# Optimization experiments

Hardware: AMD Instinct MI355X
Metric: run time of the kernel (lower is better)

The kernel has to match this reference:

```python
import jax, jax.numpy as jnp
import numpy as np

EPS = 1e-5
GROUPS = 32

def _group_norm(x, w, b):
    N, C, H, W = x.shape
    g = GROUPS
    xr = x.reshape(N, g, C // g, H, W)
    mean = xr.mean(axis=(2, 3, 4), keepdims=True)
    var = xr.var(axis=(2, 3, 4), keepdims=True)
    xn = ((xr - mean) / jnp.sqrt(var + EPS)).reshape(N, C, H, W)
    return xn * w[None, :, None, None] + b[None, :, None, None]

def setup_inputs() -> dict:
    key = jax.random.key(0)
    ks = jax.random.split(key, 9)
    N, C, H, W = 8, 256, 64, 64
    c = C // 2
    s_in = 1.0 / np.sqrt(C)
    s_out = 1.0 / np.sqrt(c)
    return {
        "x": jax.random.normal(ks[0], (N, C, H, W), dtype=jnp.float32),
        "gn_w": jnp.ones((C,), dtype=jnp.float32),
        "gn_b": jnp.zeros((C,), dtype=jnp.float32),
        "wq": jax.random.normal(ks[1], (c, C), dtype=jnp.float32) * s_in,
        "bq": jax.random.normal(ks[2], (c,), dtype=jnp.float32) * 0.01,
        "wk": jax.random.normal(ks[3], (c, C), dtype=jnp.float32) * s_in,
        "bk": jax.random.normal(ks[4], (c,), dtype=jnp.float32) * 0.01,
        "wv": jax.random.normal(ks[5], (c, C), dtype=jnp.float32) * s_in,
        "bv": jax.random.normal(ks[6], (c,), dtype=jnp.float32) * 0.01,
        "wo": jax.random.normal(ks[7], (C, c), dtype=jnp.float32) * s_out,
        "bo": jax.random.normal(ks[8], (C,), dtype=jnp.float32) * 0.01,
    }

def reference(x, gn_w, gn_b, wq, bq, wk, bk, wv, bv, wo, bo):
    N, C, H, W = x.shape
    c = C // 2
    L = H * W
    f = jax.nn.silu(_group_norm(x, gn_w, gn_b))  # [N,C,H,W]
    fv = f.reshape(N, C, L)  # [N,C,L]
    q = jnp.einsum('oc,ncl->nol', wq, fv) + bq[None, :, None]  # [N,c,L]
    k = jnp.einsum('oc,ncl->nol', wk, fv) + bk[None, :, None]
    v = jnp.einsum('oc,ncl->nol', wv, fv) + bv[None, :, None]
    e = jnp.einsum('nci,ncj->nij', q, k)          # [N,L,L] (no scaling, as in source)
    a = jax.nn.softmax(e, axis=-1)
    f2 = jnp.einsum('ncj,nij->nci', v, a)          # [N,c,L]
    out = jnp.einsum('oc,ncl->nol', wo, jax.nn.silu(f2)) + bo[None, :, None]
    return out.reshape(N, C, H, W) + x
```

## Files before the change

### kernel.cpp

```cpp
#include <hip/hip_runtime.h>

typedef _Float16 f16;
typedef _Float16 f16x8 __attribute__((ext_vector_type(8)));
typedef float f32x4 __attribute__((ext_vector_type(4)));

static constexpr int N_ = 8, C_ = 256, c_ = 128, L_ = 4096;

#define DEVI __device__ __forceinline__

DEVI f16x8 ldg8(const f16* p){ return *reinterpret_cast<const f16x8*>(p); }
DEVI f32x4 mfma16(f16x8 a, f16x8 b, f32x4 c){
  return __builtin_amdgcn_mfma_f32_16x16x32_f16(a, b, c, 0, 0, 0);
}
DEVI float silu(float x){ return x / (1.f + __expf(-x)); }

__global__ __launch_bounds__(256) void prep_weights(const float* __restrict__ wq,
    const float* __restrict__ wk, const float* __restrict__ wv,
    const float* __restrict__ wo, f16* __restrict__ dst){
  int i = blockIdx.x * 256 + threadIdx.x;
  int off = i & 32767;
  const float* s;
  switch (i >> 15){
    case 0:  s = wq; break;
    case 1:  s = wk; break;
    case 2:  s = wv; break;
    default: s = wo; break;
  }
  dst[i] = (f16)s[off];
}

__global__ __launch_bounds__(256) void gn_stats(const float* __restrict__ x,
                                                float* __restrict__ st){
  int n = blockIdx.x >> 5, g = blockIdx.x & 31;
  const float* base = x + (size_t)(n * C_ + g * 8) * L_;
  float s = 0.f, ss = 0.f;
  for (int it = 0; it < 32; ++it){
    float4 v = *reinterpret_cast<const float4*>(base + it * 1024 + threadIdx.x * 4);
    s  += v.x + v.y + v.z + v.w;
    ss += v.x * v.x + v.y * v.y + v.z * v.z + v.w * v.w;
  }
  #pragma unroll
  for (int m = 1; m <= 32; m <<= 1){ s += __shfl_xor(s, m); ss += __shfl_xor(ss, m); }
  __shared__ float red[8];
  int w = threadIdx.x >> 6;
  if ((threadIdx.x & 63) == 0){ red[w] = s; red[4 + w] = ss; }
  __syncthreads();
  if (threadIdx.x == 0){
    s  = red[0] + red[1] + red[2] + red[3];
    ss = red[4] + red[5] + red[6] + red[7];
    float mean = s * (1.f / 32768.f);
    float var  = ss * (1.f / 32768.f) - mean * mean;
    float2 o; o.x = mean; o.y = rsqrtf(var + 1e-5f);
    reinterpret_cast<float2*>(st)[blockIdx.x] = o;
  }
}

__global__ __launch_bounds__(256) void gn_apply(const float* __restrict__ x,
    const float* __restrict__ st, const float* __restrict__ gw,
    const float* __restrict__ gb, f16* __restrict__ fT){
  int n = blockIdx.z, c0 = blockIdx.y * 64, l0 = blockIdx.x * 64;
  __shared__ f16 tile[64][72];
  int t = threadIdx.x;
  int cr = t >> 4, lc = (t & 15) * 4;
  const float* xb = x + (size_t)(n * C_ + c0) * L_ + l0;
  #pragma unroll
  for (int p = 0; p < 4; ++p){
    int cc = cr + p * 16;
    int ch = c0 + cc;
    float2 ms = reinterpret_cast<const float2*>(st)[n * 32 + (ch >> 3)];
    float w = gw[ch], b = gb[ch];
    float4 v = *reinterpret_cast<const float4*>(xb + (size_t)cc * L_ + lc);
    float f0 = (v.x - ms.x) * ms.y * w + b;
    float f1 = (v.y - ms.x) * ms.y * w + b;
    float f2 = (v.z - ms.x) * ms.y * w + b;
    float f3 = (v.w - ms.x) * ms.y * w + b;
    tile[cc][lc + 0] = (f16)silu(f0);
    tile[cc][lc + 1] = (f16)silu(f1);
    tile[cc][lc + 2] = (f16)silu(f2);
    tile[cc][lc + 3] = (f16)silu(f3);
  }
  __syncthreads();
  int lr = t >> 2, cq = (t & 3) * 16;
  f16 tmp[16];
  #pragma unroll
  for (int e = 0; e < 16; ++e) tmp[e] = tile[cq + e][lr];
  f16* o = fT + (size_t)(n * L_ + l0 + lr) * C_ + c0 + cq;
  *reinterpret_cast<f16x8*>(o)     = *reinterpret_cast<f16x8*>(tmp);
  *reinterpret_cast<f16x8*>(o + 8) = *reinterpret_cast<f16x8*>(tmp + 8);
}

template<int EPI>
__global__ __launch_bounds__(256) void proj(const f16* __restrict__ A, size_t a_nstr,
    const f16* __restrict__ B, size_t b_nstr, const float* __restrict__ bias,
    void* __restrict__ outv, size_t o_nstr, int ldo,
    const float* __restrict__ resid, size_t r_nstr, int Ks,
    const float* __restrict__ bias2, void* __restrict__ outv2){
  int n = blockIdx.z;
  int i0 = blockIdx.x * 64;
  int w  = threadIdx.x >> 6;
  int jw = blockIdx.y * 128 + w * 32;
  int lane = threadIdx.x & 63, l15 = lane & 15, g4 = lane >> 4;
  const f16* Ab = A + (size_t)n * a_nstr;
  const f16* Bb = B + (size_t)n * b_nstr;
  int K = Ks * 32;
  f32x4 acc[4][2];
  #pragma unroll
  for (int mf = 0; mf < 4; ++mf)
    #pragma unroll
    for (int nf = 0; nf < 2; ++nf) acc[mf][nf] = (f32x4){0.f, 0.f, 0.f, 0.f};

  for (int ks = 0; ks < Ks; ++ks){
    int kk = ks * 32 + 8 * g4;
    f16x8 a[4], b[2];
    #pragma unroll
    for (int mf = 0; mf < 4; ++mf)
      a[mf] = ldg8(Ab + (size_t)(i0 + 16 * mf + l15) * K + kk);
    #pragma unroll
    for (int nf = 0; nf < 2; ++nf)
      b[nf] = ldg8(Bb + (size_t)(jw + 16 * nf + l15) * K + kk);
    #pragma unroll
    for (int mf = 0; mf < 4; ++mf)
      #pragma unroll
      for (int nf = 0; nf < 2; ++nf)
        acc[mf][nf] = mfma16(a[mf], b[nf], acc[mf][nf]);
  }

  #pragma unroll
  for (int mf = 0; mf < 4; ++mf){
    #pragma unroll
    for (int nf = 0; nf < 2; ++nf){
      int j = jw + 16 * nf + l15;
      #pragma unroll
      for (int r = 0; r < 4; ++r){
        int i = i0 + 16 * mf + 4 * g4 + r;
        float v = acc[mf][nf][r];
        if (EPI == 1){
          ((f16*)outv)[(size_t)n * o_nstr + (size_t)i * ldo + j] = (f16)(v + bias[i]);
        } else if (EPI == 2){
          size_t oidx = (size_t)n * o_nstr + (size_t)i * ldo + j;
          ((float*)outv)[oidx] = v + bias[i] + resid[(size_t)n * r_nstr + (size_t)i * ldo + j];
        } else {
          if (j < 128)
            ((f16*)outv)[(size_t)n * o_nstr + (size_t)i * ldo + j] = (f16)(v + bias[j]);
          else
            ((f16*)outv2)[(size_t)n * o_nstr + (size_t)i * ldo + (j - 128)] = (f16)(v + bias2[j - 128]);
        }
      }
    }
  }
}

__global__ __launch_bounds__(256) void flash(const f16* __restrict__ Qg,
    const f16* __restrict__ Kg, const f16* __restrict__ Vg, f16* __restrict__ Og){
  __shared__ char Ksh[16384];
  __shared__ char Vsh[16384];
  __shared__ char Psh[8192];
  int n = blockIdx.y;
  int q0 = blockIdx.x * 64;
  int tid = threadIdx.x;
  int w = tid >> 6, lane = tid & 63, l15 = lane & 15, g4 = lane >> 4;
  int qb = q0 + w * 16;

  const f16* Qn = Qg + (size_t)n * L_ * 128;
  const f16* Kn = Kg + (size_t)n * L_ * 128;
  const f16* Vn = Vg + (size_t)n * 128 * L_;

  f16x8 qf[4];
  #pragma unroll
  for (int ks = 0; ks < 4; ++ks)
    qf[ks] = ldg8(Qn + (size_t)(qb + l15) * 128 + ks * 32 + 8 * g4);

  f32x4 o[8];
  #pragma unroll
  for (int nf = 0; nf < 8; ++nf) o[nf] = (f32x4){0.f, 0.f, 0.f, 0.f};
  float mrow[4], lrow[4];
  #pragma unroll
  for (int r = 0; r < 4; ++r){ mrow[r] = -1e30f; lrow[r] = 0.f; }

  for (int t = 0; t < 64; ++t){
    #pragma unroll
    for (int it = 0; it < 4; ++it){
      int cid = it * 256 + tid;
      int j = cid >> 4, c16 = cid & 15;
      float4 val = *reinterpret_cast<const float4*>(Kn + (size_t)(t * 64 + j) * 128 + c16 * 8);
      *reinterpret_cast<float4*>(Ksh + j * 256 + ((c16 * 16) ^ ((j & 7) << 4))) = val;
    }
    #pragma unroll
    for (int it = 0; it < 4; ++it){
      int cid = it * 256 + tid;
      int d = cid >> 3, c16 = cid & 7;
      float4 val = *reinterpret_cast<const float4*>(Vn + (size_t)d * L_ + t * 64 + c16 * 8);
      *reinterpret_cast<float4*>(Vsh + d * 128 + ((c16 * 16) ^ ((d & 7) << 4))) = val;
    }
    __syncthreads();

    f32x4 s[4];
    #pragma unroll
    for (int nf = 0; nf < 4; ++nf) s[nf] = (f32x4){0.f, 0.f, 0.f, 0.f};
    #pragma unroll
    for (int ks = 0; ks < 4; ++ks){
      #pragma unroll
      for (int nf = 0; nf < 4; ++nf){
        int j = 16 * nf + l15;
        f16x8 kf = *reinterpret_cast<const f16x8*>(Ksh + j * 256 + ((64 * ks + 16 * g4) ^ ((j & 7) << 4)));
        s[nf] = mfma16(qf[ks], kf, s[nf]);
      }
    }

    float scl[4];
    #pragma unroll
    for (int r = 0; r < 4; ++r){
      float pm = fmaxf(fmaxf(s[0][r], s[1][r]), fmaxf(s[2][r], s[3][r]));
      pm = fmaxf(pm, __shfl_xor(pm, 1));
      pm = fmaxf(pm, __shfl_xor(pm, 2));
      pm = fmaxf(pm, __shfl_xor(pm, 4));
      pm = fmaxf(pm, __shfl_xor(pm, 8));
      float mnew = fmaxf(mrow[r], pm);
      scl[r] = __expf(mrow[r] - mnew);
      mrow[r] = mnew;
    }
    #pragma unroll
    for (int nf = 0; nf < 4; ++nf)
      #pragma unroll
      for (int r = 0; r < 4; ++r)
        s[nf][r] = __expf(s[nf][r] - mrow[r]);
    #pragma unroll
    for (int r = 0; r < 4; ++r){
      float rs = s[0][r] + s[1][r] + s[2][r] + s[3][r];
      rs += __shfl_xor(rs, 1);
      rs += __shfl_xor(rs, 2);
      rs += __shfl_xor(rs, 4);
      rs += __shfl_xor(rs, 8);
      lrow[r] = lrow[r] * scl[r] + rs;
    }
    #pragma unroll
    for (int nf = 0; nf < 8; ++nf)
      #pragma unroll
      for (int r = 0; r < 4; ++r)
        o[nf][r] *= scl[r];

    char* pb = Psh + w * 2048;
    #pragma unroll
    for (int nf = 0; nf < 4; ++nf)
      #pragma unroll
      for (int r = 0; r < 4; ++r){
        int i = 4 * g4 + r;
        int jj = 16 * nf + l15;
        *reinterpret_cast<f16*>(pb + i * 128 + ((2 * jj) ^ ((i & 7) << 4))) = (f16)s[nf][r];
      }

    #pragma unroll
    for (int ks = 0; ks < 2; ++ks){
      f16x8 pa = *reinterpret_cast<const f16x8*>(pb + l15 * 128 + ((64 * ks + 16 * g4) ^ ((l15 & 7) << 4)));
      #pragma unroll
      for (int nf = 0; nf < 8; ++nf){
        int d = 16 * nf + l15;
        f16x8 vf = *reinterpret_cast<const f16x8*>(Vsh + d * 128 + ((64 * ks + 16 * g4) ^ ((d & 7) << 4)));
        o[nf] = mfma16(pa, vf, o[nf]);
      }
    }
    __syncthreads();
  }

  f16* Ob = Og + (size_t)n * L_ * 128;
  #pragma unroll
  for (int r = 0; r < 4; ++r){
    float inv = 1.f / lrow[r];
    #pragma unroll
    for (int nf = 0; nf < 8; ++nf){
      float val = o[nf][r] * inv;
      Ob[(size_t)(qb + 4 * g4 + r) * 128 + 16 * nf + l15] = (f16)silu(val);
    }
  }
}

extern "C" void kernel_launch(void* const* d_in, const int* in_sizes, int n_in,
                              void* d_out, int out_size, void* d_ws, size_t ws_size,
                              hipStream_t stream){
  const float* x   = (const float*)d_in[0];
  const float* gnw = (const float*)d_in[1];
  const float* gnb = (const float*)d_in[2];
  const float* wq  = (const float*)d_in[3];
  const float* bq  = (const float*)d_in[4];
  const float* wk  = (const float*)d_in[5];
  const float* bk  = (const float*)d_in[6];
  const float* wv  = (const float*)d_in[7];
  const float* bv  = (const float*)d_in[8];
  const float* wo  = (const float*)d_in[9];
  const float* bo  = (const float*)d_in[10];
  float* out = (float*)d_out;

  char* ws = (char*)d_ws;
  f16* fT   = (f16*)(ws);
  f16* q    = (f16*)(ws + ((size_t)16 << 20));
  f16* k    = (f16*)(ws + ((size_t)24 << 20));
  f16* v    = (f16*)(ws + ((size_t)32 << 20));
  f16* gbuf = (f16*)(ws + ((size_t)40 << 20));
  f16* wh   = (f16*)(ws + ((size_t)48 << 20));
  float* st = (float*)(ws + ((size_t)49 << 20));

  prep_weights<<<512, 256, 0, stream>>>(wq, wk, wv, wo, wh);
  gn_stats<<<256, 256, 0, stream>>>(x, st);
  gn_apply<<<dim3(64, 4, 8), 256, 0, stream>>>(x, st, gnw, gnb, fT);

  proj<3><<<dim3(64, 2, 8), 256, 0, stream>>>(fT, (size_t)L_ * C_, wh, 0, bq,
                                              q, (size_t)L_ * c_, c_, nullptr, 0, 8, bk, k);
  proj<1><<<dim3(2, 32, 8), 256, 0, stream>>>(wh + 65536, 0, fT, (size_t)L_ * C_, bv,
                                              v, (size_t)c_ * L_, L_, nullptr, 0, 8, nullptr, nullptr);
  flash<<<dim3(64, 8), 256, 0, stream>>>(q, k, v, gbuf);
  proj<2><<<dim3(4, 32, 8), 256, 0, stream>>>(wh + 98304, 0, gbuf, (size_t)L_ * c_, bo,
                                              out, (size_t)C_ * L_, L_, x, (size_t)C_ * L_, 4, nullptr, nullptr);
}
```

Before: 341.3 us.

## Prefetch K/V tiles into registers and add lazy softmax rescaling in attention

```diff
diff --git a/kernel.cpp b/kernel.cpp
--- a/kernel.cpp
+++ b/kernel.cpp
@@ -173,26 +173,47 @@
   f32x4 o[8];
   #pragma unroll
   for (int nf = 0; nf < 8; ++nf) o[nf] = (f32x4){0.f, 0.f, 0.f, 0.f};
-  float mrow[4], lrow[4];
-  #pragma unroll
-  for (int r = 0; r < 4; ++r){ mrow[r] = -1e30f; lrow[r] = 0.f; }
+  float mrow[4], lpart[4];
+  #pragma unroll
+  for (int r = 0; r < 4; ++r){ mrow[r] = -1e30f; lpart[r] = 0.f; }
+
+  float4 kreg[4], vreg[4];
+  #pragma unroll
+  for (int it = 0; it < 4; ++it){
+    int cid = it * 256 + tid; int j = cid >> 4, c = cid & 15;
+    kreg[it] = *reinterpret_cast<const float4*>(Kn + (size_t)j * 128 + c * 8);
+  }
+  #pragma unroll
+  for (int it = 0; it < 4; ++it){
+    int cid = it * 256 + tid; int d = cid >> 3, c = cid & 7;
+    vreg[it] = *reinterpret_cast<const float4*>(Vn + (size_t)d * L_ + c * 8);
+  }
 
   for (int t = 0; t < 64; ++t){
     #pragma unroll
     for (int it = 0; it < 4; ++it){
-      int cid = it * 256 + tid;
-      int j = cid >> 4, c16 = cid & 15;
-      float4 val = *reinterpret_cast<const float4*>(Kn + (size_t)(t * 64 + j) * 128 + c16 * 8);
-      *reinterpret_cast<float4*>(Ksh + j * 256 + ((c16 * 16) ^ ((j & 7) << 4))) = val;
+      int cid = it * 256 + tid; int j = cid >> 4, c = cid & 15;
+      *reinterpret_cast<float4*>(Ksh + j * 256 + ((c * 16) ^ ((j & 7) << 4))) = kreg[it];
     }
     #pragma unroll
     for (int it = 0; it < 4; ++it){
-      int cid = it * 256 + tid;
-      int d = cid >> 3, c16 = cid & 7;
-      float4 val = *reinterpret_cast<const float4*>(Vn + (size_t)d * L_ + t * 64 + c16 * 8);
-      *reinterpret_cast<float4*>(Vsh + d * 128 + ((c16 * 16) ^ ((d & 7) << 4))) = val;
+      int cid = it * 256 + tid; int d = cid >> 3, c = cid & 7;
+      *reinterpret_cast<float4*>(Vsh + d * 128 + ((c * 16) ^ ((d & 7) << 4))) = vreg[it];
     }
     __syncthreads();
+
+    if (t + 1 < 64){
+      #pragma unroll
+      for (int it = 0; it < 4; ++it){
+        int cid = it * 256 + tid; int j = cid >> 4, c = cid & 15;
+        kreg[it] = *reinterpret_cast<const float4*>(Kn + (size_t)((t + 1) * 64 + j) * 128 + c * 8);
+      }
+      #pragma unroll
+      for (int it = 0; it < 4; ++it){
+        int cid = it * 256 + tid; int d = cid >> 3, c = cid & 7;
+        vreg[it] = *reinterpret_cast<const float4*>(Vn + (size_t)d * L_ + (t + 1) * 64 + c * 8);
+      }
+    }
 
     f32x4 s[4];
     #pragma unroll
@@ -207,17 +228,27 @@
       }
     }
 
-    float scl[4];
-    #pragma unroll
-    for (int r = 0; r < 4; ++r){
-      float pm = fmaxf(fmaxf(s[0][r], s[1][r]), fmaxf(s[2][r], s[3][r]));
-      pm = fmaxf(pm, __shfl_xor(pm, 1));
-      pm = fmaxf(pm, __shfl_xor(pm, 2));
-      pm = fmaxf(pm, __shfl_xor(pm, 4));
-      pm = fmaxf(pm, __shfl_xor(pm, 8));
-      float mnew = fmaxf(mrow[r], pm);
-      scl[r] = __expf(mrow[r] - mnew);
-      mrow[r] = mnew;
+    float pm[4];
+    #pragma unroll
+    for (int r = 0; r < 4; ++r)
+      pm[r] = fmaxf(fmaxf(s[0][r], s[1][r]), fmaxf(s[2][r], s[3][r]));
+    bool ex = (pm[0] > mrow[0] + 8.f) | (pm[1] > mrow[1] + 8.f) |
+              (pm[2] > mrow[2] + 8.f) | (pm[3] > mrow[3] + 8.f);
+    if (__any(ex)){
+      #pragma unroll
+      for (int r = 0; r < 4; ++r){
+        float m = pm[r];
+        m = fmaxf(m, __shfl_xor(m, 1));
+        m = fmaxf(m, __shfl_xor(m, 2));
+        m = fmaxf(m, __shfl_xor(m, 4));
+        m = fmaxf(m, __shfl_xor(m, 8));
+        float mn = fmaxf(mrow[r], m);
+        float sc = __expf(mrow[r] - mn);
+        mrow[r] = mn;
+        lpart[r] *= sc;
+        #pragma unroll
+        for (int nf = 0; nf < 8; ++nf) o[nf][r] *= sc;
+      }
     }
     #pragma unroll
     for (int nf = 0; nf < 4; ++nf)
@@ -225,19 +256,8 @@
       for (int r = 0; r < 4; ++r)
         s[nf][r] = __expf(s[nf][r] - mrow[r]);
     #pragma unroll
-    for (int r = 0; r < 4; ++r){
-      float rs = s[0][r] + s[1][r] + s[2][r] + s[3][r];
-      rs += __shfl_xor(rs, 1);
-      rs += __shfl_xor(rs, 2);
-      rs += __shfl_xor(rs, 4);
-      rs += __shfl_xor(rs, 8);
-      lrow[r] = lrow[r] * scl[r] + rs;
-    }
-    #pragma unroll
-    for (int nf = 0; nf < 8; ++nf)
-      #pragma unroll
-      for (int r = 0; r < 4; ++r)
-        o[nf][r] *= scl[r];
+    for (int r = 0; r < 4; ++r)
+      lpart[r] += (s[0][r] + s[1][r]) + (s[2][r] + s[3][r]);
 
     char* pb = Psh + w * 2048;
     #pragma unroll
@@ -262,6 +282,16 @@
     __syncthreads();
   }
 
+  float lrow[4];
+  #pragma unroll
+  for (int r = 0; r < 4; ++r){
+    float rs = lpart[r];
+    rs += __shfl_xor(rs, 1);
+    rs += __shfl_xor(rs, 2);
+    rs += __shfl_xor(rs, 4);
+    rs += __shfl_xor(rs, 8);
+    lrow[r] = rs;
+  }
   f16* Ob = Og + (size_t)n * L_ * 128;
   #pragma unroll
   for (int r = 0; r < 4; ++r){
```

Result: slower. 553.5 us (+62.2%).
